# Kernel tuning notes

Measured on AMD Instinct MI355X. Metric: run time of the kernel, lower is better.

The kernel has to match this reference:

```python
import jax, jax.numpy as jnp
import numpy as np

EPS_BN = 1e-5

def conv1(W, x):
    # 1x1 conv1d, no bias: W (Cout,Cin), x (B,Cin,N)
    return jnp.einsum('oc,bcn->bon', W, x)

def bn(x, g, b):
    # training-mode BatchNorm1d over (batch, points) per channel
    m = jnp.mean(x, axis=(0, 2), keepdims=True)
    v = jnp.mean((x - m) ** 2, axis=(0, 2), keepdims=True)
    return g[None, :, None] * (x - m) / jnp.sqrt(v + EPS_BN) + b[None, :, None]

def three_interpolation(p_dense, p_sparse, f_sparse):
    # p_dense (B,N1,3), p_sparse (B,N2,3), f_sparse (B,C,N2) -> (B,C,N1)
    d2 = jnp.sum((p_dense[:, :, None, :] - p_sparse[:, None, :, :]) ** 2, axis=-1)  # (B,N1,N2)
    neg, idx = jax.lax.top_k(-d2, 3)  # 3 nearest neighbors, (B,N1,3)
    w = 1.0 / (jnp.maximum(-neg, 0.0) + 1e-8)  # inverse (squared) distance, as pointnet2 three_nn
    w = w / jnp.sum(w, axis=-1, keepdims=True)
    gathered = jax.vmap(lambda f, i: f[:, i])(f_sparse, idx)  # (B,C,N1,3)
    return jnp.einsum('bcnk,bnk->bcn', gathered, w)

def fp(p_dense, f_skip, p_sparse, f_sparse, W1, g1, b1, W2, g2, b2):
    # FeaturePropogation upsample branch: concat(skip, interp) -> [conv1d+BN] x decoder_layers (act_args=None)
    x = jnp.concatenate([f_skip, three_interpolation(p_dense, p_sparse, f_sparse)], axis=1)
    x = bn(conv1(W1, x), g1, b1)
    x = bn(conv1(W2, x), g2, b2)
    return x

def setup_inputs():
    key = jax.random.key(0)
    ks = iter(jax.random.split(key, 40))
    B, N = 4, 8192
    Ns = [N, N, 2048, 512, 128]      # point counts of p0..p4 (strides 4)
    Cs = [128, 256, 512, 1024]       # encoder_channel_list
    d = {}
    for i in range(5):
        d[f'p{i}'] = jax.random.normal(next(ks), (B, Ns[i], 3), jnp.float32)
    for i in range(4):
        d[f'f{i + 1}'] = jax.random.normal(next(ks), (B, Cs[i], Ns[i + 1]), jnp.float32)
    d['cls_label'] = jax.random.randint(next(ks), (B, 1), 0, 16)
    # class-label convs: 16 -> 64 (BN+GELU) -> C0
    d['Wc1'] = jax.random.normal(next(ks), (64, 16), jnp.float32) * 0.1
    d['gc'] = jax.random.uniform(next(ks), (64,), jnp.float32, 0.5, 1.5)
    d['bc'] = jax.random.normal(next(ks), (64,), jnp.float32) * 0.1
    d['Wc2'] = jax.random.normal(next(ks), (Cs[0], 64), jnp.float32) * 0.1
    # decoder stages, coarsest (s2) to finest (s0)
    ins = [Cs[2] + Cs[3], Cs[1] + Cs[2], Cs[0] + Cs[1]]
    outs = [Cs[2], Cs[1], Cs[0]]
    for tag, ci, co in zip(['s2', 's1', 's0'], ins, outs):
        d[f'W{tag}a'] = jax.random.normal(next(ks), (co, ci), jnp.float32) * 0.05
        d[f'g{tag}a'] = jax.random.uniform(next(ks), (co,), jnp.float32, 0.5, 1.5)
        d[f'b{tag}a'] = jax.random.normal(next(ks), (co,), jnp.float32) * 0.1
        d[f'W{tag}b'] = jax.random.normal(next(ks), (co, co), jnp.float32) * 0.05
        d[f'g{tag}b'] = jax.random.uniform(next(ks), (co,), jnp.float32, 0.5, 1.5)
        d[f'b{tag}b'] = jax.random.normal(next(ks), (co,), jnp.float32) * 0.1
    return d

def reference(p0, p1, p2, p3, p4, f1, f2, f3, f4, cls_label,
              Wc1, gc, bc, Wc2,
              Ws2a, gs2a, bs2a, Ws2b, gs2b, bs2b,
              Ws1a, gs1a, bs1a, Ws1b, gs1b, bs1b,
              Ws0a, gs0a, bs0a, Ws0b, gs0b, bs0b):
    B, N = p0.shape[0], p0.shape[1]
    # one-hot class embedding broadcast over points, mapped 16 -> 64 -> C0
    one_hot = jax.nn.one_hot(cls_label[:, 0], 16, dtype=f1.dtype)  # (B,16)
    cls_feat = jnp.broadcast_to(one_hot[:, :, None], (B, 16, N))
    cls_feat = conv1(Wc2, jax.nn.gelu(bn(conv1(Wc1, cls_feat), gc, bc), approximate=False))
    # decoder stages, coarse to fine
    f3n = fp(p3, f3, p4, f4, Ws2a, gs2a, bs2a, Ws2b, gs2b, bs2b)   # (B,512,512)
    f2n = fp(p2, f2, p3, f3n, Ws1a, gs1a, bs1a, Ws1b, gs1b, bs1b)  # (B,256,2048)
    f1n = fp(p1, f1 + cls_feat, p2, f2n, Ws0a, gs0a, bs0a, Ws0b, gs0b, bs0b)  # (B,128,8192)
    return f1n
```

## Files before the change

### kernel.cpp

```cpp
#include <hip/hip_runtime.h>
#include <math.h>

#define BN_EPS 1e-5f

typedef float f32x4 __attribute__((ext_vector_type(4)));
typedef short s16x8 __attribute__((ext_vector_type(8)));
typedef short s16x4 __attribute__((ext_vector_type(4)));

__device__ __forceinline__ unsigned short f2bf(float f) {
    unsigned u = __builtin_bit_cast(unsigned, f);
    u = u + 0x7FFFu + ((u >> 16) & 1u);
    return (unsigned short)(u >> 16);
}
__device__ __forceinline__ float bf2f(unsigned short s) {
    unsigned u = ((unsigned)s) << 16;
    return __builtin_bit_cast(float, u);
}

__device__ __forceinline__ void gload16(const void* g, void* l) {
    __builtin_amdgcn_global_load_lds((const __attribute__((address_space(1))) unsigned int*)g,
                                     (__attribute__((address_space(3))) unsigned int*)l,
                                     16, 0, 0);
}

__global__ __launch_bounds__(512) void cls_kernel(const int* __restrict__ lbl,
                                                  const float* __restrict__ Wc1,
                                                  const float* __restrict__ gc,
                                                  const float* __restrict__ bc,
                                                  const float* __restrict__ Wc2,
                                                  float* __restrict__ cls_vec) {
    __shared__ float h[4 * 64];
    __shared__ float act[4 * 64];
    int tid = threadIdx.x;
    if (tid < 256) {
        int b = tid >> 6, c = tid & 63;
        h[b * 64 + c] = Wc1[c * 16 + lbl[b]];
    }
    __syncthreads();
    if (tid < 64) {
        int c = tid;
        float m = 0.f;
        for (int b = 0; b < 4; b++) m += h[b * 64 + c];
        m *= 0.25f;
        float v = 0.f;
        for (int b = 0; b < 4; b++) { float d = h[b * 64 + c] - m; v += d * d; }
        v *= 0.25f;
        float sc = gc[c] * rsqrtf(v + BN_EPS);
        float sh = bc[c] - m * sc;
        for (int b = 0; b < 4; b++) {
            float x = h[b * 64 + c] * sc + sh;
            act[b * 64 + c] = 0.5f * x * (1.f + erff(x * 0.70710678118654752f));
        }
    }
    __syncthreads();
    int b = tid >> 7, o = tid & 127;
    float s = 0.f;
    for (int c = 0; c < 64; c++) s += Wc2[o * 64 + c] * act[b * 64 + c];
    cls_vec[b * 128 + o] = s;
}

__global__ __launch_bounds__(256) void transpose_cp(const float* __restrict__ in,
                                                    unsigned short* __restrict__ out,
                                                    const float* __restrict__ addv,
                                                    int C, int N) {
    __shared__ float t[32][33];
    int b = blockIdx.z;
    int n0 = blockIdx.x * 32, c0 = blockIdx.y * 32;
    int i = threadIdx.x & 31, jj = threadIdx.x >> 5;
#pragma unroll
    for (int j = jj; j < 32; j += 8) {
        float v = in[((size_t)b * C + c0 + j) * N + n0 + i];
        if (addv) v += addv[b * C + c0 + j];
        t[j][i] = v;
    }
    __syncthreads();
    int j2 = threadIdx.x & 31, i2b = threadIdx.x >> 5;
#pragma unroll
    for (int i2 = i2b; i2 < 32; i2 += 8)
        out[((size_t)b * N + n0 + i2) * C + c0 + j2] = f2bf(t[j2][i2]);
}

__global__ __launch_bounds__(256) void knn_kernel(const float* __restrict__ pd,
                                                  const float* __restrict__ ps,
                                                  int N1, int N2,
                                                  int* __restrict__ idx,
                                                  float* __restrict__ w) {
    __shared__ float spx[2048], spy[2048], spz[2048];
    int b = blockIdx.y;
    int tid = threadIdx.x;
    for (int t = tid; t < N2; t += 256) {
        size_t base = ((size_t)b * N2 + t) * 3;
        spx[t] = ps[base];
        spy[t] = ps[base + 1];
        spz[t] = ps[base + 2];
    }
    __syncthreads();
    int sub = tid & 7;
    int n = blockIdx.x * 32 + (tid >> 3);
    size_t pb = ((size_t)b * N1 + n) * 3;
    float px = pd[pb], py = pd[pb + 1], pz = pd[pb + 2];
    float d0 = 3.4e38f, d1 = 3.4e38f, d2 = 3.4e38f;
    int i0 = 0, i1 = 0, i2 = 0;
#pragma unroll 4
    for (int j = sub; j < N2; j += 8) {
        float dx = px - spx[j], dy = py - spy[j], dz = pz - spz[j];
        float d = dx * dx + dy * dy + dz * dz;
        bool c2 = d < d2;
        float nd = c2 ? d : d2;  int ni = c2 ? j : i2;
        bool c1 = nd < d1;
        float t1 = c1 ? nd : d1; int ti1 = c1 ? ni : i1;
        float t2 = c1 ? d1 : nd; int ti2 = c1 ? i1 : ni;
        bool c0 = t1 < d0;
        d2 = t2; i2 = ti2;
        d1 = c0 ? d0 : t1; i1 = c0 ? i0 : ti1;
        d0 = c0 ? t1 : d0; i0 = c0 ? ti1 : i0;
    }
    unsigned long long k0 = ((unsigned long long)__builtin_bit_cast(unsigned, d0) << 32) | (unsigned)i0;
    unsigned long long k1 = ((unsigned long long)__builtin_bit_cast(unsigned, d1) << 32) | (unsigned)i1;
    unsigned long long k2 = ((unsigned long long)__builtin_bit_cast(unsigned, d2) << 32) | (unsigned)i2;
#pragma unroll
    for (int m = 1; m < 8; m <<= 1) {
        unsigned long long e0, e1, e2;
        { int lo = __shfl_xor((int)(unsigned)(k0 & 0xFFFFFFFFull), m), hi = __shfl_xor((int)(unsigned)(k0 >> 32), m);
          e0 = ((unsigned long long)(unsigned)hi << 32) | (unsigned)lo; }
        { int lo = __shfl_xor((int)(unsigned)(k1 & 0xFFFFFFFFull), m), hi = __shfl_xor((int)(unsigned)(k1 >> 32), m);
          e1 = ((unsigned long long)(unsigned)hi << 32) | (unsigned)lo; }
        { int lo = __shfl_xor((int)(unsigned)(k2 & 0xFFFFFFFFull), m), hi = __shfl_xor((int)(unsigned)(k2 >> 32), m);
          e2 = ((unsigned long long)(unsigned)hi << 32) | (unsigned)lo; }
        unsigned long long t0, t1;
        t0 = k0 > e0 ? k0 : e0; k0 = k0 < e0 ? k0 : e0; t1 = k1 > t0 ? k1 : t0; k1 = k1 < t0 ? k1 : t0; k2 = k2 < t1 ? k2 : t1;
        t0 = k0 > e1 ? k0 : e1; k0 = k0 < e1 ? k0 : e1; t1 = k1 > t0 ? k1 : t0; k1 = k1 < t0 ? k1 : t0; k2 = k2 < t1 ? k2 : t1;
        t0 = k0 > e2 ? k0 : e2; k0 = k0 < e2 ? k0 : e2; t1 = k1 > t0 ? k1 : t0; k1 = k1 < t0 ? k1 : t0; k2 = k2 < t1 ? k2 : t1;
    }
    if (sub == 0) {
        float f0 = __builtin_bit_cast(float, (unsigned)(k0 >> 32));
        float f1 = __builtin_bit_cast(float, (unsigned)(k1 >> 32));
        float f2 = __builtin_bit_cast(float, (unsigned)(k2 >> 32));
        float w0 = 1.f / (f0 + 1e-8f), w1 = 1.f / (f1 + 1e-8f), w2 = 1.f / (f2 + 1e-8f);
        float s = 1.f / (w0 + w1 + w2);
        size_t o = ((size_t)b * N1 + n) * 3;
        idx[o] = (int)(unsigned)(k0 & 0xFFFFFFFFull);
        idx[o + 1] = (int)(unsigned)(k1 & 0xFFFFFFFFull);
        idx[o + 2] = (int)(unsigned)(k2 & 0xFFFFFFFFull);
        w[o] = w0 * s; w[o + 1] = w1 * s; w[o + 2] = w2 * s;
    }
}

__global__ __launch_bounds__(256) void build_x(const unsigned short* __restrict__ skipT,
                                               const unsigned short* __restrict__ fsT,
                                               const int* __restrict__ idx,
                                               const float* __restrict__ w,
                                               unsigned short* __restrict__ x,
                                               int Cskip, int Ctot, int Csp, int N1, int N2) {
    int cq = Ctot >> 2;
    size_t gid = (size_t)blockIdx.x * 256 + threadIdx.x;
    if (gid >= (size_t)4 * N1 * cq) return;
    int c = (int)(gid % cq) * 4;
    int n = (int)((gid / cq) % N1);
    int b = (int)(gid / ((size_t)cq * N1));
    s16x4 o;
    if (c < Cskip) {
        o = *(const s16x4*)(skipT + ((size_t)b * N1 + n) * Cskip + c);
    } else {
        int c2 = c - Cskip;
        size_t ob = ((size_t)b * N1 + n) * 3;
        int i0 = idx[ob], i1 = idx[ob + 1], i2 = idx[ob + 2];
        float w0 = w[ob], w1 = w[ob + 1], w2 = w[ob + 2];
        const unsigned short* f0 = fsT + ((size_t)b * N2 + i0) * Csp + c2;
        const unsigned short* f1 = fsT + ((size_t)b * N2 + i1) * Csp + c2;
        const unsigned short* f2 = fsT + ((size_t)b * N2 + i2) * Csp + c2;
        s16x4 v0 = *(const s16x4*)f0, v1 = *(const s16x4*)f1, v2 = *(const s16x4*)f2;
#pragma unroll
        for (int j = 0; j < 4; j++) {
            float v = w0 * bf2f((unsigned short)v0[j]) + w1 * bf2f((unsigned short)v1[j]) + w2 * bf2f((unsigned short)v2[j]);
            o[j] = (short)f2bf(v);
        }
    }
    *(s16x4*)(x + ((size_t)b * N1 + n) * Ctot + c) = o;
}

__global__ __launch_bounds__(256) void wprep(const float* __restrict__ W,
                                             const float* __restrict__ sc,
                                             const float* __restrict__ sh,
                                             unsigned short* __restrict__ Wb,
                                             float* __restrict__ bias,
                                             int K, int kStart) {
    int m = blockIdx.x;
    int tid = threadIdx.x;
    float bsum = 0.f;
    for (int k = tid; k < K; k += 256) {
        float wv = W[(size_t)m * K + k];
        float o = wv;
        if (sc && k >= kStart) {
            o = wv * sc[k - kStart];
            bsum += wv * sh[k - kStart];
        }
        Wb[(size_t)m * K + k] = f2bf(o);
    }
    __shared__ float ls[256];
    ls[tid] = bsum;
    __syncthreads();
    for (int o = 128; o > 0; o >>= 1) {
        if (tid < o) ls[tid] += ls[tid + o];
        __syncthreads();
    }
    if (tid == 0) bias[m] = ls[0];
}

__global__ __launch_bounds__(256) void gemm64(const unsigned short* __restrict__ XT,
                                              const unsigned short* __restrict__ Wb,
                                              const float* __restrict__ bias,
                                              unsigned short* __restrict__ OutT,
                                              float* __restrict__ ps,
                                              int BN, int K, int M) {
    __shared__ unsigned short As[2][64 * 32];
    __shared__ unsigned short Bs[2][64 * 32];
    __shared__ float sred[2][2][32][2];
    int tid = threadIdx.x;
    int lane = tid & 63, wid = tid >> 6;
    int wn = wid & 1, wm = wid >> 1;
    int bx = blockIdx.x, by = blockIdx.y;

    int srow = (wid << 4) + (lane >> 2);
    int skcol = (lane & 3) << 3;
    const unsigned short* gA = XT + (size_t)(bx * 64 + srow) * K + skcol;
    const unsigned short* gB = Wb + (size_t)(by * 64 + srow) * K + skcol;

    f32x4 acc[2][2];
#pragma unroll
    for (int i = 0; i < 2; i++)
#pragma unroll
        for (int j = 0; j < 2; j++) acc[i][j] = (f32x4)0.f;

    int nt = K >> 5;
    gload16(gA, &As[0][wid * 512]);
    gload16(gB, &Bs[0][wid * 512]);

    int r16 = lane & 15, q = lane >> 4;
    for (int t = 0; t < nt; t++) {
        int cur = t & 1;
        if (t + 1 < nt) {
            int k0 = (t + 1) << 5;
            gload16(gA + k0, &As[cur ^ 1][wid * 512]);
            gload16(gB + k0, &Bs[cur ^ 1][wid * 512]);
            asm volatile("s_waitcnt vmcnt(2)" ::: "memory");
        } else {
            asm volatile("s_waitcnt vmcnt(0)" ::: "memory");
        }
        __syncthreads();
        s16x8 afr[2], bfr[2];
        afr[0] = *(const s16x8*)&As[cur][(wn * 32 + r16) * 32 + q * 8];
        afr[1] = *(const s16x8*)&As[cur][(wn * 32 + 16 + r16) * 32 + q * 8];
        bfr[0] = *(const s16x8*)&Bs[cur][(wm * 32 + r16) * 32 + q * 8];
        bfr[1] = *(const s16x8*)&Bs[cur][(wm * 32 + 16 + r16) * 32 + q * 8];
        asm volatile("s_waitcnt lgkmcnt(0)" ::: "memory");
        __builtin_amdgcn_sched_barrier(0);
        __syncthreads();
#pragma unroll
        for (int i = 0; i < 2; i++)
#pragma unroll
            for (int j = 0; j < 2; j++)
                acc[i][j] = __builtin_amdgcn_mfma_f32_16x16x32_bf16(afr[i], bfr[j], acc[i][j], 0, 0, 0);
    }

    int mc0 = by * 64 + wm * 32 + r16;
    float bv[2] = { bias[mc0], bias[mc0 + 16] };
    unsigned short* Ob = OutT + (size_t)(bx * 64) * M + by * 64;
    float s[2] = {0.f, 0.f}, qq[2] = {0.f, 0.f};
#pragma unroll
    for (int i = 0; i < 2; i++) {
#pragma unroll
        for (int j = 0; j < 2; j++) {
            int mcol = wm * 32 + j * 16 + r16;
#pragma unroll
            for (int r = 0; r < 4; r++) {
                float v = acc[i][j][r] + bv[j];
                s[j] += v; qq[j] += v * v;
                int n = wn * 32 + i * 16 + q * 4 + r;
                Ob[(size_t)n * M + mcol] = f2bf(v);
            }
        }
    }
#pragma unroll
    for (int j = 0; j < 2; j++) {
        s[j] += __shfl_xor(s[j], 16); s[j] += __shfl_xor(s[j], 32);
        qq[j] += __shfl_xor(qq[j], 16); qq[j] += __shfl_xor(qq[j], 32);
    }
    if (lane < 16) {
#pragma unroll
        for (int j = 0; j < 2; j++) {
            sred[wn][wm][j * 16 + lane][0] = s[j];
            sred[wn][wm][j * 16 + lane][1] = qq[j];
        }
    }
    __syncthreads();
    if (tid < 64) {
        int wmm = tid >> 5, c = tid & 31;
        float ssum = sred[0][wmm][c][0] + sred[1][wmm][c][0];
        float qsum = sred[0][wmm][c][1] + sred[1][wmm][c][1];
        size_t blin = (size_t)by * gridDim.x + bx;
        ps[blin * 128 + tid * 2] = ssum;
        ps[blin * 128 + tid * 2 + 1] = qsum;
    }
}

__global__ __launch_bounds__(256) void bn_finalize(const float* __restrict__ ps,
                                                   const float* __restrict__ g,
                                                   const float* __restrict__ bb,
                                                   float* __restrict__ sc,
                                                   float* __restrict__ sh,
                                                   int gx, int Npts) {
    int m = blockIdx.x;
    int by = m >> 6, ch = m & 63;
    float s = 0.f, q = 0.f;
    for (int bxi = threadIdx.x; bxi < gx; bxi += 256) {
        size_t blin = (size_t)by * gx + bxi;
        s += ps[blin * 128 + ch * 2];
        q += ps[blin * 128 + ch * 2 + 1];
    }
    __shared__ float ls[256], lq[256];
    ls[threadIdx.x] = s; lq[threadIdx.x] = q;
    __syncthreads();
    for (int o = 128; o > 0; o >>= 1) {
        if (threadIdx.x < o) { ls[threadIdx.x] += ls[threadIdx.x + o]; lq[threadIdx.x] += lq[threadIdx.x + o]; }
        __syncthreads();
    }
    if (threadIdx.x == 0) {
        float inv = 1.f / (float)Npts;
        float mean = ls[0] * inv;
        float var = fmaxf(lq[0] * inv - mean * mean, 0.f);
        float scale = g[m] * rsqrtf(var + BN_EPS);
        sc[m] = scale;
        sh[m] = bb[m] - mean * scale;
    }
}

__global__ __launch_bounds__(256) void out_bn_tr(const unsigned short* __restrict__ in,
                                                 float* __restrict__ out,
                                                 const float* __restrict__ sc,
                                                 const float* __restrict__ sh,
                                                 int M, int N) {
    __shared__ float t[32][33];
    int b = blockIdx.z;
    int n0 = blockIdx.x * 32, m0 = blockIdx.y * 32;
    int j = threadIdx.x & 31, ii = threadIdx.x >> 5;
#pragma unroll
    for (int i = ii; i < 32; i += 8)
        t[i][j] = bf2f(in[((size_t)b * N + n0 + i) * M + m0 + j]);
    __syncthreads();
    int i2 = threadIdx.x & 31, j2b = threadIdx.x >> 5;
#pragma unroll
    for (int j2 = j2b; j2 < 32; j2 += 8)
        out[((size_t)b * M + m0 + j2) * N + n0 + i2] = t[i2][j2] * sc[m0 + j2] + sh[m0 + j2];
}

extern "C" void kernel_launch(void* const* d_in, const int* in_sizes, int n_in,
                              void* d_out, int out_size, void* d_ws, size_t ws_size,
                              hipStream_t stream) {
    const float* p1 = (const float*)d_in[1];
    const float* p2 = (const float*)d_in[2];
    const float* p3 = (const float*)d_in[3];
    const float* p4 = (const float*)d_in[4];
    const float* f1 = (const float*)d_in[5];
    const float* f2 = (const float*)d_in[6];
    const float* f3 = (const float*)d_in[7];
    const float* f4 = (const float*)d_in[8];
    const int* cls = (const int*)d_in[9];
    const float* Wc1 = (const float*)d_in[10];
    const float* gc  = (const float*)d_in[11];
    const float* bc  = (const float*)d_in[12];
    const float* Wc2 = (const float*)d_in[13];
    const float* Ws2a = (const float*)d_in[14];
    const float* gs2a = (const float*)d_in[15];
    const float* bs2a = (const float*)d_in[16];
    const float* Ws2b = (const float*)d_in[17];
    const float* gs2b = (const float*)d_in[18];
    const float* bs2b = (const float*)d_in[19];
    const float* Ws1a = (const float*)d_in[20];
    const float* gs1a = (const float*)d_in[21];
    const float* bs1a = (const float*)d_in[22];
    const float* Ws1b = (const float*)d_in[23];
    const float* gs1b = (const float*)d_in[24];
    const float* bs1b = (const float*)d_in[25];
    const float* Ws0a = (const float*)d_in[26];
    const float* gs0a = (const float*)d_in[27];
    const float* bs0a = (const float*)d_in[28];
    const float* Ws0b = (const float*)d_in[29];
    const float* gs0b = (const float*)d_in[30];
    const float* bs0b = (const float*)d_in[31];

    char* ws = (char*)d_ws;
    size_t off = 0;
    auto alloc = [&](size_t bytes) { char* p = ws + off; off += (bytes + 255) & ~(size_t)255; return p; };
    unsigned short* F4T = (unsigned short*)alloc((size_t)4 * 128 * 1024 * 2);
    unsigned short* F3T = (unsigned short*)alloc((size_t)4 * 512 * 512 * 2);
    unsigned short* F2T = (unsigned short*)alloc((size_t)4 * 2048 * 256 * 2);
    unsigned short* F1T = (unsigned short*)alloc((size_t)4 * 8192 * 128 * 2);
    unsigned short* XS  = (unsigned short*)alloc((size_t)4 * 8192 * 384 * 2);
    unsigned short* YA  = (unsigned short*)alloc((size_t)4 * 8192 * 128 * 2);
    unsigned short* FN2 = (unsigned short*)alloc((size_t)4 * 512 * 512 * 2);
    unsigned short* FN1 = (unsigned short*)alloc((size_t)4 * 2048 * 256 * 2);
    unsigned short* XO  = (unsigned short*)alloc((size_t)4 * 8192 * 128 * 2);
    unsigned short* WB2a = (unsigned short*)alloc((size_t)512 * 1536 * 2);
    unsigned short* WB2b = (unsigned short*)alloc((size_t)512 * 512 * 2);
    unsigned short* WB1a = (unsigned short*)alloc((size_t)256 * 768 * 2);
    unsigned short* WB1b = (unsigned short*)alloc((size_t)256 * 256 * 2);
    unsigned short* WB0a = (unsigned short*)alloc((size_t)128 * 384 * 2);
    unsigned short* WB0b = (unsigned short*)alloc((size_t)128 * 128 * 2);
    float* BI2a = (float*)alloc(512 * 4); float* BI2b = (float*)alloc(512 * 4);
    float* BI1a = (float*)alloc(256 * 4); float* BI1b = (float*)alloc(256 * 4);
    float* BI0a = (float*)alloc(128 * 4); float* BI0b = (float*)alloc(128 * 4);
    int*   IDX = (int*)alloc((size_t)4 * 8192 * 3 * 4);
    float* WGT = (float*)alloc((size_t)4 * 8192 * 3 * 4);
    float* CLSV = (float*)alloc(4 * 128 * 4);
    float* PS = (float*)alloc((size_t)1024 * 128 * 4);
    float* SC2a = (float*)alloc(512 * 4); float* SH2a = (float*)alloc(512 * 4);
    float* SC2b = (float*)alloc(512 * 4); float* SH2b = (float*)alloc(512 * 4);
    float* SC1a = (float*)alloc(512 * 4); float* SH1a = (float*)alloc(512 * 4);
    float* SC1b = (float*)alloc(512 * 4); float* SH1b = (float*)alloc(512 * 4);
    float* SC0a = (float*)alloc(512 * 4); float* SH0a = (float*)alloc(512 * 4);
    float* SC0b = (float*)alloc(512 * 4); float* SH0b = (float*)alloc(512 * 4);
    float* OUT = (float*)d_out;

    cls_kernel<<<1, 512, 0, stream>>>(cls, Wc1, gc, bc, Wc2, CLSV);
    transpose_cp<<<dim3(128 / 32, 1024 / 32, 4), 256, 0, stream>>>(f4, F4T, nullptr, 1024, 128);
    transpose_cp<<<dim3(512 / 32, 512 / 32, 4), 256, 0, stream>>>(f3, F3T, nullptr, 512, 512);
    transpose_cp<<<dim3(2048 / 32, 256 / 32, 4), 256, 0, stream>>>(f2, F2T, nullptr, 256, 2048);
    transpose_cp<<<dim3(8192 / 32, 128 / 32, 4), 256, 0, stream>>>(f1, F1T, CLSV, 128, 8192);

    wprep<<<512, 256, 0, stream>>>(Ws2a, nullptr, nullptr, WB2a, BI2a, 1536, 0);
    knn_kernel<<<dim3(512 / 32, 4), 256, 0, stream>>>(p3, p4, 512, 128, IDX, WGT);
    build_x<<<(int)(((size_t)4 * 512 * (1536 / 4) + 255) / 256), 256, 0, stream>>>(
        F3T, F4T, IDX, WGT, XS, 512, 1536, 1024, 512, 128);
    gemm64<<<dim3(32, 8), 256, 0, stream>>>(XS, WB2a, BI2a, YA, PS, 2048, 1536, 512);
    bn_finalize<<<512, 256, 0, stream>>>(PS, gs2a, bs2a, SC2a, SH2a, 32, 2048);
    wprep<<<512, 256, 0, stream>>>(Ws2b, SC2a, SH2a, WB2b, BI2b, 512, 0);
    gemm64<<<dim3(32, 8), 256, 0, stream>>>(YA, WB2b, BI2b, FN2, PS, 2048, 512, 512);
    bn_finalize<<<512, 256, 0, stream>>>(PS, gs2b, bs2b, SC2b, SH2b, 32, 2048);

    wprep<<<256, 256, 0, stream>>>(Ws1a, SC2b, SH2b, WB1a, BI1a, 768, 256);
    knn_kernel<<<dim3(2048 / 32, 4), 256, 0, stream>>>(p2, p3, 2048, 512, IDX, WGT);
    build_x<<<(int)(((size_t)4 * 2048 * (768 / 4) + 255) / 256), 256, 0, stream>>>(
        F2T, FN2, IDX, WGT, XS, 256, 768, 512, 2048, 512);
    gemm64<<<dim3(128, 4), 256, 0, stream>>>(XS, WB1a, BI1a, YA, PS, 8192, 768, 256);
    bn_finalize<<<256, 256, 0, stream>>>(PS, gs1a, bs1a, SC1a, SH1a, 128, 8192);
    wprep<<<256, 256, 0, stream>>>(Ws1b, SC1a, SH1a, WB1b, BI1b, 256, 0);
    gemm64<<<dim3(128, 4), 256, 0, stream>>>(YA, WB1b, BI1b, FN1, PS, 8192, 256, 256);
    bn_finalize<<<256, 256, 0, stream>>>(PS, gs1b, bs1b, SC1b, SH1b, 128, 8192);

    wprep<<<128, 256, 0, stream>>>(Ws0a, SC1b, SH1b, WB0a, BI0a, 384, 128);
    knn_kernel<<<dim3(8192 / 32, 4), 256, 0, stream>>>(p1, p2, 8192, 2048, IDX, WGT);
    build_x<<<(int)(((size_t)4 * 8192 * (384 / 4) + 255) / 256), 256, 0, stream>>>(
        F1T, FN1, IDX, WGT, XS, 128, 384, 256, 8192, 2048);
    gemm64<<<dim3(512, 2), 256, 0, stream>>>(XS, WB0a, BI0a, YA, PS, 32768, 384, 128);
    bn_finalize<<<128, 256, 0, stream>>>(PS, gs0a, bs0a, SC0a, SH0a, 512, 32768);
    wprep<<<128, 256, 0, stream>>>(Ws0b, SC0a, SH0a, WB0b, BI0b, 128, 0);
    gemm64<<<dim3(512, 2), 256, 0, stream>>>(YA, WB0b, BI0b, XO, PS, 32768, 128, 128);
    bn_finalize<<<128, 256, 0, stream>>>(PS, gs0b, bs0b, SC0b, SH0b, 512, 32768);

    out_bn_tr<<<dim3(8192 / 32, 128 / 32, 4), 256, 0, stream>>>(XO, OUT, SC0b, SH0b, 128, 8192);
}
```

Before: 220.2 us.

## Batch transposes and KNN into single launches, vectorize KNN and build_x

Merges the class-embedding kernel and four transposes into one launch, with each f1 tile block recomputing the class vector locally. Merges the three KNN searches into one launch with separate index/weight buffers. Each thread now scans a contiguous padded LDS chunk with float4 loads and a med3-based top-3 update. build_x widens to 8 bf16 per thread. The goal is fewer launches and serialization points and cheaper inner loops, at the cost of redundant class-vector computation in many blocks.

```diff
diff --git a/kernel.cpp b/kernel.cpp
--- a/kernel.cpp
+++ b/kernel.cpp
@@ -23,101 +23,118 @@
                                      16, 0, 0);
 }
 
-__global__ __launch_bounds__(512) void cls_kernel(const int* __restrict__ lbl,
-                                                  const float* __restrict__ Wc1,
-                                                  const float* __restrict__ gc,
-                                                  const float* __restrict__ bc,
-                                                  const float* __restrict__ Wc2,
-                                                  float* __restrict__ cls_vec) {
-    __shared__ float h[4 * 64];
-    __shared__ float act[4 * 64];
+__global__ __launch_bounds__(256) void tr_all(const float* __restrict__ f1,
+                                              const float* __restrict__ f2,
+                                              const float* __restrict__ f3,
+                                              const float* __restrict__ f4,
+                                              unsigned short* __restrict__ F1T,
+                                              unsigned short* __restrict__ F2T,
+                                              unsigned short* __restrict__ F3T,
+                                              unsigned short* __restrict__ F4T,
+                                              const int* __restrict__ lbl,
+                                              const float* __restrict__ Wc1,
+                                              const float* __restrict__ gc,
+                                              const float* __restrict__ bc,
+                                              const float* __restrict__ Wc2) {
+    __shared__ float t[32][33];
+    __shared__ float clsv[32];
+    __shared__ float hsh[4][64];
+    __shared__ float actsh[4][64];
+    int bx = blockIdx.x, b = blockIdx.y;
+    const float* in; unsigned short* out; int C, N, nx, seg; bool docls = false;
+    if (bx < 128)      { in = f4; out = F4T; C = 1024; N = 128;  nx = 4;   seg = bx; }
+    else if (bx < 384) { in = f3; out = F3T; C = 512;  N = 512;  nx = 16;  seg = bx - 128; }
+    else if (bx < 896) { in = f2; out = F2T; C = 256;  N = 2048; nx = 64;  seg = bx - 384; }
+    else               { in = f1; out = F1T; C = 128;  N = 8192; nx = 256; seg = bx - 896; docls = true; }
+    int n0 = (seg % nx) * 32, c0 = (seg / nx) * 32;
     int tid = threadIdx.x;
-    if (tid < 256) {
-        int b = tid >> 6, c = tid & 63;
-        h[b * 64 + c] = Wc1[c * 16 + lbl[b]];
-    }
-    __syncthreads();
-    if (tid < 64) {
-        int c = tid;
-        float m = 0.f;
-        for (int b = 0; b < 4; b++) m += h[b * 64 + c];
-        m *= 0.25f;
-        float v = 0.f;
-        for (int b = 0; b < 4; b++) { float d = h[b * 64 + c] - m; v += d * d; }
-        v *= 0.25f;
-        float sc = gc[c] * rsqrtf(v + BN_EPS);
-        float sh = bc[c] - m * sc;
-        for (int b = 0; b < 4; b++) {
-            float x = h[b * 64 + c] * sc + sh;
-            act[b * 64 + c] = 0.5f * x * (1.f + erff(x * 0.70710678118654752f));
-        }
-    }
-    __syncthreads();
-    int b = tid >> 7, o = tid & 127;
-    float s = 0.f;
-    for (int c = 0; c < 64; c++) s += Wc2[o * 64 + c] * act[b * 64 + c];
-    cls_vec[b * 128 + o] = s;
-}
-
-__global__ __launch_bounds__(256) void transpose_cp(const float* __restrict__ in,
-                                                    unsigned short* __restrict__ out,
-                                                    const float* __restrict__ addv,
-                                                    int C, int N) {
-    __shared__ float t[32][33];
-    int b = blockIdx.z;
-    int n0 = blockIdx.x * 32, c0 = blockIdx.y * 32;
-    int i = threadIdx.x & 31, jj = threadIdx.x >> 5;
+    if (docls) {
+        { int b2 = tid >> 6, c = tid & 63; hsh[b2][c] = Wc1[c * 16 + lbl[b2]]; }
+        __syncthreads();
+        if (tid < 64) {
+            int c = tid;
+            float m = 0.f;
+            for (int b2 = 0; b2 < 4; b2++) m += hsh[b2][c];
+            m *= 0.25f;
+            float v = 0.f;
+            for (int b2 = 0; b2 < 4; b2++) { float d = hsh[b2][c] - m; v += d * d; }
+            v *= 0.25f;
+            float sc = gc[c] * rsqrtf(v + BN_EPS);
+            float sh = bc[c] - m * sc;
+            for (int b2 = 0; b2 < 4; b2++) {
+                float x = hsh[b2][c] * sc + sh;
+                actsh[b2][c] = 0.5f * x * (1.f + erff(x * 0.70710678118654752f));
+            }
+        }
+        __syncthreads();
+        if (tid < 32) {
+            float s = 0.f;
+            for (int c = 0; c < 64; c++) s += Wc2[(size_t)(c0 + tid) * 64 + c] * actsh[b][c];
+            clsv[tid] = s;
+        }
+        __syncthreads();
+    }
+    int i = tid & 31, jj = tid >> 5;
 #pragma unroll
     for (int j = jj; j < 32; j += 8) {
         float v = in[((size_t)b * C + c0 + j) * N + n0 + i];
-        if (addv) v += addv[b * C + c0 + j];
+        if (docls) v += clsv[j];
         t[j][i] = v;
     }
     __syncthreads();
-    int j2 = threadIdx.x & 31, i2b = threadIdx.x >> 5;
+    int j2 = tid & 31, i2b = tid >> 5;
 #pragma unroll
     for (int i2 = i2b; i2 < 32; i2 += 8)
         out[((size_t)b * N + n0 + i2) * C + c0 + j2] = f2bf(t[j2][i2]);
 }
 
-__global__ __launch_bounds__(256) void knn_kernel(const float* __restrict__ pd,
-                                                  const float* __restrict__ ps,
-                                                  int N1, int N2,
-                                                  int* __restrict__ idx,
-                                                  float* __restrict__ w) {
-    __shared__ float spx[2048], spy[2048], spz[2048];
-    int b = blockIdx.y;
+template<int N2, int CHUNK, int STRIDE>
+__device__ __forceinline__ void knn_body(const float* __restrict__ pd,
+                                         const float* __restrict__ ps,
+                                         int N1, int grp, int b,
+                                         int* __restrict__ idx, float* __restrict__ w,
+                                         float* spx, float* spy, float* spz) {
     int tid = threadIdx.x;
-    for (int t = tid; t < N2; t += 256) {
-        size_t base = ((size_t)b * N2 + t) * 3;
-        spx[t] = ps[base];
-        spy[t] = ps[base + 1];
-        spz[t] = ps[base + 2];
+    for (int g = tid; g < N2; g += 256) {
+        int s = g / CHUNK, off = g % CHUNK;
+        size_t base = ((size_t)b * N2 + g) * 3;
+        spx[s * STRIDE + off] = ps[base];
+        spy[s * STRIDE + off] = ps[base + 1];
+        spz[s * STRIDE + off] = ps[base + 2];
     }
     __syncthreads();
     int sub = tid & 7;
-    int n = blockIdx.x * 32 + (tid >> 3);
+    int n = grp * 32 + (tid >> 3);
     size_t pb = ((size_t)b * N1 + n) * 3;
     float px = pd[pb], py = pd[pb + 1], pz = pd[pb + 2];
-    float d0 = 3.4e38f, d1 = 3.4e38f, d2 = 3.4e38f;
-    int i0 = 0, i1 = 0, i2 = 0;
-#pragma unroll 4
-    for (int j = sub; j < N2; j += 8) {
-        float dx = px - spx[j], dy = py - spy[j], dz = pz - spz[j];
-        float d = dx * dx + dy * dy + dz * dz;
-        bool c2 = d < d2;
-        float nd = c2 ? d : d2;  int ni = c2 ? j : i2;
-        bool c1 = nd < d1;
-        float t1 = c1 ? nd : d1; int ti1 = c1 ? ni : i1;
-        float t2 = c1 ? d1 : nd; int ti2 = c1 ? i1 : ni;
-        bool c0 = t1 < d0;
-        d2 = t2; i2 = ti2;
-        d1 = c0 ? d0 : t1; i1 = c0 ? i0 : ti1;
-        d0 = c0 ? t1 : d0; i0 = c0 ? ti1 : i0;
-    }
-    unsigned long long k0 = ((unsigned long long)__builtin_bit_cast(unsigned, d0) << 32) | (unsigned)i0;
-    unsigned long long k1 = ((unsigned long long)__builtin_bit_cast(unsigned, d1) << 32) | (unsigned)i1;
-    unsigned long long k2 = ((unsigned long long)__builtin_bit_cast(unsigned, d2) << 32) | (unsigned)i2;
+    float dd0 = 3.4e38f, dd1 = 3.4e38f, dd2 = 3.4e38f;
+    int ii0 = 0, ii1 = 0, ii2 = 0;
+    const float* rx = spx + sub * STRIDE;
+    const float* ry = spy + sub * STRIDE;
+    const float* rz = spz + sub * STRIDE;
+    int jbase = sub * CHUNK;
+    for (int t = 0; t < CHUNK; t += 4) {
+        f32x4 x4 = *(const f32x4*)(rx + t);
+        f32x4 y4 = *(const f32x4*)(ry + t);
+        f32x4 z4 = *(const f32x4*)(rz + t);
+#pragma unroll
+        for (int e = 0; e < 4; e++) {
+            float dx = px - x4[e], dy = py - y4[e], dz = pz - z4[e];
+            float d = dx * dx + dy * dy + dz * dz;
+            int j = jbase + t + e;
+            bool C0 = d < dd0, C1 = d < dd1, C2 = d < dd2;
+            int ni2 = C1 ? ii1 : (C2 ? j : ii2);
+            int ni1 = C0 ? ii0 : (C1 ? j : ii1);
+            int ni0 = C0 ? j : ii0;
+            dd2 = __builtin_amdgcn_fmed3f(d, dd1, dd2);
+            dd1 = __builtin_amdgcn_fmed3f(d, dd0, dd1);
+            dd0 = fminf(d, dd0);
+            ii0 = ni0; ii1 = ni1; ii2 = ni2;
+        }
+    }
+    unsigned long long k0 = ((unsigned long long)__builtin_bit_cast(unsigned, dd0) << 32) | (unsigned)ii0;
+    unsigned long long k1 = ((unsigned long long)__builtin_bit_cast(unsigned, dd1) << 32) | (unsigned)ii1;
+    unsigned long long k2 = ((unsigned long long)__builtin_bit_cast(unsigned, dd2) << 32) | (unsigned)ii2;
 #pragma unroll
     for (int m = 1; m < 8; m <<= 1) {
         unsigned long long e0, e1, e2;
@@ -146,37 +163,50 @@
     }
 }
 
+__global__ __launch_bounds__(256) void knn_all(const float* __restrict__ p1,
+                                               const float* __restrict__ p2,
+                                               const float* __restrict__ p3,
+                                               const float* __restrict__ p4,
+                                               int* __restrict__ idx0, float* __restrict__ w0,
+                                               int* __restrict__ idx1, float* __restrict__ w1,
+                                               int* __restrict__ idx2, float* __restrict__ w2) {
+    __shared__ float spx[8 * 264], spy[8 * 264], spz[8 * 264];
+    int bx = blockIdx.x, b = blockIdx.y;
+    if (bx < 16)      knn_body<128, 16, 24>(p3, p4, 512, bx, b, idx2, w2, spx, spy, spz);
+    else if (bx < 80) knn_body<512, 64, 72>(p2, p3, 2048, bx - 16, b, idx1, w1, spx, spy, spz);
+    else              knn_body<2048, 256, 264>(p1, p2, 8192, bx - 80, b, idx0, w0, spx, spy, spz);
+}
+
 __global__ __launch_bounds__(256) void build_x(const unsigned short* __restrict__ skipT,
                                                const unsigned short* __restrict__ fsT,
                                                const int* __restrict__ idx,
                                                const float* __restrict__ w,
                                                unsigned short* __restrict__ x,
                                                int Cskip, int Ctot, int Csp, int N1, int N2) {
-    int cq = Ctot >> 2;
+    int cq = Ctot >> 3;
     size_t gid = (size_t)blockIdx.x * 256 + threadIdx.x;
     if (gid >= (size_t)4 * N1 * cq) return;
-    int c = (int)(gid % cq) * 4;
+    int c = (int)(gid % cq) * 8;
     int n = (int)((gid / cq) % N1);
     int b = (int)(gid / ((size_t)cq * N1));
-    s16x4 o;
+    s16x8 o;
     if (c < Cskip) {
-        o = *(const s16x4*)(skipT + ((size_t)b * N1 + n) * Cskip + c);
+        o = *(const s16x8*)(skipT + ((size_t)b * N1 + n) * Cskip + c);
     } else {
         int c2 = c - Cskip;
         size_t ob = ((size_t)b * N1 + n) * 3;
         int i0 = idx[ob], i1 = idx[ob + 1], i2 = idx[ob + 2];
         float w0 = w[ob], w1 = w[ob + 1], w2 = w[ob + 2];
-        const unsigned short* f0 = fsT + ((size_t)b * N2 + i0) * Csp + c2;
-        const unsigned short* f1 = fsT + ((size_t)b * N2 + i1) * Csp + c2;
-        const unsigned short* f2 = fsT + ((size_t)b * N2 + i2) * Csp + c2;
-        s16x4 v0 = *(const s16x4*)f0, v1 = *(const s16x4*)f1, v2 = *(const s16x4*)f2;
-#pragma unroll
-        for (int j = 0; j < 4; j++) {
+        s16x8 v0 = *(const s16x8*)(fsT + ((size_t)b * N2 + i0) * Csp + c2);
+        s16x8 v1 = *(const s16x8*)(fsT + ((size_t)b * N2 + i1) * Csp + c2);
+        s16x8 v2 = *(const s16x8*)(fsT + ((size_t)b * N2 + i2) * Csp + c2);
+#pragma unroll
+        for (int j = 0; j < 8; j++) {
             float v = w0 * bf2f((unsigned short)v0[j]) + w1 * bf2f((unsigned short)v1[j]) + w2 * bf2f((unsigned short)v2[j]);
             o[j] = (short)f2bf(v);
         }
     }
-    *(s16x4*)(x + ((size_t)b * N1 + n) * Ctot + c) = o;
+    *(s16x8*)(x + ((size_t)b * N1 + n) * Ctot + c) = o;
 }
 
 __global__ __launch_bounds__(256) void wprep(const float* __restrict__ W,
@@ -410,9 +440,12 @@
     float* BI2a = (float*)alloc(512 * 4); float* BI2b = (float*)alloc(512 * 4);
     float* BI1a = (float*)alloc(256 * 4); float* BI1b = (float*)alloc(256 * 4);
     float* BI0a = (float*)alloc(128 * 4); float* BI0b = (float*)alloc(128 * 4);
-    int*   IDX = (int*)alloc((size_t)4 * 8192 * 3 * 4);
-    float* WGT = (float*)alloc((size_t)4 * 8192 * 3 * 4);
-    float* CLSV = (float*)alloc(4 * 128 * 4);
+    int*   IDX0 = (int*)alloc((size_t)4 * 8192 * 3 * 4);
+    float* WGT0 = (float*)alloc((size_t)4 * 8192 * 3 * 4);
+    int*   IDX1 = (int*)alloc((size_t)4 * 2048 * 3 * 4);
+    float* WGT1 = (float*)alloc((size_t)4 * 2048 * 3 * 4);
+    int*   IDX2 = (int*)alloc((size_t)4 * 512 * 3 * 4);
+    float* WGT2 = (float*)alloc((size_t)4 * 512 * 3 * 4);
     float* PS = (float*)alloc((size_t)1024 * 128 * 4);
     float* SC2a = (float*)alloc(512 * 4); float* SH2a = (float*)alloc(512 * 4);
     float* SC2b = (float*)alloc(512 * 4); float* SH2b = (float*)alloc(512 * 4);
@@ -422,16 +455,12 @@
     float* SC0b = (float*)alloc(512 * 4); float* SH0b = (float*)alloc(512 * 4);
     float* OUT = (float*)d_out;
 
-    cls_kernel<<<1, 512, 0, stream>>>(cls, Wc1, gc, bc, Wc2, CLSV);
-    transpose_cp<<<dim3(128 / 32, 1024 / 32, 4), 256, 0, stream>>>(f4, F4T, nullptr, 1024, 128);
-    transpose_cp<<<dim3(512 / 32, 512 / 32, 4), 256, 0, stream>>>(f3, F3T, nullptr, 512, 512);
-    transpose_cp<<<dim3(2048 / 32, 256 / 32, 4), 256, 0, stream>>>(f2, F2T, nullptr, 256, 2048);
-    transpose_cp<<<dim3(8192 / 32, 128 / 32, 4), 256, 0, stream>>>(f1, F1T, CLSV, 128, 8192);
+    tr_all<<<dim3(1920, 4), 256, 0, stream>>>(f1, f2, f3, f4, F1T, F2T, F3T, F4T, cls, Wc1, gc, bc, Wc2);
+    knn_all<<<dim3(336, 4), 256, 0, stream>>>(p1, p2, p3, p4, IDX0, WGT0, IDX1, WGT1, IDX2, WGT2);
 
     wprep<<<512, 256, 0, stream>>>(Ws2a, nullptr, nullptr, WB2a, BI2a, 1536, 0);
-    knn_kernel<<<dim3(512 / 32, 4), 256, 0, stream>>>(p3, p4, 512, 128, IDX, WGT);
-    build_x<<<(int)(((size_t)4 * 512 * (1536 / 4) + 255) / 256), 256, 0, stream>>>(
-        F3T, F4T, IDX, WGT, XS, 512, 1536, 1024, 512, 128);
+    build_x<<<(int)(((size_t)4 * 512 * (1536 / 8) + 255) / 256), 256, 0, stream>>>(
+        F3T, F4T, IDX2, WGT2, XS, 512, 1536, 1024, 512, 128);
     gemm64<<<dim3(32, 8), 256, 0, stream>>>(XS, WB2a, BI2a, YA, PS, 2048, 1536, 512);
     bn_finalize<<<512, 256, 0, stream>>>(PS, gs2a, bs2a, SC2a, SH2a, 32, 2048);
     wprep<<<512, 256, 0, stream>>>(Ws2b, SC2a, SH2a, WB2b, BI2b, 512, 0);
@@ -439,9 +468,8 @@
     bn_finalize<<<512, 256, 0, stream>>>(PS, gs2b, bs2b, SC2b, SH2b, 32, 2048);
 
     wprep<<<256, 256, 0, stream>>>(Ws1a, SC2b, SH2b, WB1a, BI1a, 768, 256);
-    knn_kernel<<<dim3(2048 / 32, 4), 256, 0, stream>>>(p2, p3, 2048, 512, IDX, WGT);
-    build_x<<<(int)(((size_t)4 * 2048 * (768 / 4) + 255) / 256), 256, 0, stream>>>(
-        F2T, FN2, IDX, WGT, XS, 256, 768, 512, 2048, 512);
+    build_x<<<(int)(((size_t)4 * 2048 * (768 / 8) + 255) / 256), 256, 0, stream>>>(
+        F2T, FN2, IDX1, WGT1, XS, 256, 768, 512, 2048, 512);
     gemm64<<<dim3(128, 4), 256, 0, stream>>>(XS, WB1a, BI1a, YA, PS, 8192, 768, 256);
     bn_finalize<<<256, 256, 0, stream>>>(PS, gs1a, bs1a, SC1a, SH1a, 128, 8192);
     wprep<<<256, 256, 0, stream>>>(Ws1b, SC1a, SH1a, WB1b, BI1b, 256, 0);
@@ -449,9 +477,8 @@
     bn_finalize<<<256, 256, 0, stream>>>(PS, gs1b, bs1b, SC1b, SH1b, 128, 8192);
 
     wprep<<<128, 256, 0, stream>>>(Ws0a, SC1b, SH1b, WB0a, BI0a, 384, 128);
-    knn_kernel<<<dim3(8192 / 32, 4), 256, 0, stream>>>(p1, p2, 8192, 2048, IDX, WGT);
-    build_x<<<(int)(((size_t)4 * 8192 * (384 / 4) + 255) / 256), 256, 0, stream>>>(
-        F1T, FN1, IDX, WGT, XS, 128, 384, 256, 8192, 2048);
+    build_x<<<(int)(((size_t)4 * 8192 * (384 / 8) + 255) / 256), 256, 0, stream>>>(
+        F1T, FN1, IDX0, WGT0, XS, 128, 384, 256, 8192, 2048);
     gemm64<<<dim3(512, 2), 256, 0, stream>>>(XS, WB0a, BI0a, YA, PS, 32768, 384, 128);
     bn_finalize<<<128, 256, 0, stream>>>(PS, gs0a, bs0a, SC0a, SH0a, 512, 32768);
     wprep<<<128, 256, 0, stream>>>(Ws0b, SC0a, SH0a, WB0b, BI0b, 128, 0);
```

After: 200.0 us. 9.2% less time.
